# Optimization experiments

Hardware: AMD Instinct MI355X
Metric: run time of the kernel (lower is better)

The kernel has to match this reference:

```python
import jax, jax.numpy as jnp
import numpy as np

LM_DIM = 4096
V_DIM = 1024
N_V = 32
FF = 1024
IN_DIM = V_DIM * N_V + LM_DIM  # 36864
B = 16
T = 2048


def setup_inputs() -> dict:
    key = jax.random.key(0)
    ks = jax.random.split(key, 16)
    grd_hidden = jax.random.normal(ks[0], (T, LM_DIM), dtype=jnp.float32)
    vision_features = jax.random.normal(ks[1], (B, N_V, V_DIM), dtype=jnp.float32)
    token_batch_idx = jnp.sort(jax.random.randint(ks[2], (T,), 0, B, dtype=jnp.int64))
    def lin(k, fan_in, fan_out):
        kw, kb = jax.random.split(k)
        scale = jnp.sqrt(2.0 / (fan_in + fan_out)).astype(jnp.float32)
        W = jax.random.normal(kw, (fan_in, fan_out), dtype=jnp.float32) * scale
        b = jnp.zeros((fan_out,), dtype=jnp.float32)
        return W, b
    W1, b1 = lin(ks[3], IN_DIM, FF)
    W2, b2 = lin(ks[4], FF, FF)
    W3, b3 = lin(ks[5], FF, FF)
    W4, b4 = lin(ks[6], FF, FF)
    W5, b5 = lin(ks[7], FF, 6)
    return {"grd_hidden": grd_hidden, "vision_features": vision_features,
            "token_batch_idx": token_batch_idx,
            "W1": W1, "b1": b1, "W2": W2, "b2": b2, "W3": W3, "b3": b3,
            "W4": W4, "b4": b4, "W5": W5, "b5": b5}


def reference(grd_hidden, vision_features, token_batch_idx,
              W1, b1, W2, b2, W3, b3, W4, b4, W5, b5):
    # flatten vision latents per sample: [B, N_V*V_DIM]
    vis_flat = vision_features.reshape(vision_features.shape[0], -1)
    # per-token gather of the sample's vision feature: [T, N_V*V_DIM]
    vis_per_tok = vis_flat[token_batch_idx]
    # concat(vision, language) per token, then shared 5-layer MLP
    x = jnp.concatenate([vis_per_tok, grd_hidden], axis=-1)  # [T, IN_DIM]
    h = jax.nn.relu(x @ W1 + b1)
    h = jax.nn.relu(h @ W2 + b2)
    h = jax.nn.relu(h @ W3 + b3)
    h = jax.nn.relu(h @ W4 + b4)
    return h @ W5 + b5  # [T, 6]
```

## Files before the change

### kernel.cpp

```cpp
#include <hip/hip_runtime.h>


typedef __attribute__((ext_vector_type(8))) short bf16x8;
typedef __attribute__((ext_vector_type(4))) float f32x4;

#define LM_DIM 4096
#define FF     1024
#define VIS_K  32768
#define NB     16
#define NTOK   2048

__device__ __forceinline__ unsigned short f2bf(float f) {
    unsigned int u = __float_as_uint(f);
    u += 0x7fffu + ((u >> 16) & 1u);
    return (unsigned short)(u >> 16);
}
__device__ __forceinline__ float bf2f(unsigned short s) {
    return __uint_as_float(((unsigned int)s) << 16);
}

__device__ __forceinline__ void gload_lds16(const void* g, void* lds) {
    __builtin_amdgcn_global_load_lds(
        (const __attribute__((address_space(1))) unsigned int*)g,
        (__attribute__((address_space(3))) unsigned int*)lds,
        16, 0, 0);
}

__global__ __launch_bounds__(1024) void vis_partial(
    const float* __restrict__ W1, const float* __restrict__ vis,
    float* __restrict__ pb)
{
    const int n  = threadIdx.x;
    const int ks = blockIdx.x;
    const int k0 = ks * 128;
    __shared__ float sv[NB][128];
    for (int idx = threadIdx.x; idx < NB * 128; idx += 1024) {
        int b = idx >> 7, kk = idx & 127;
        sv[b][kk] = vis[(size_t)b * VIS_K + k0 + kk];
    }
    __syncthreads();
    float acc[NB];
#pragma unroll
    for (int b = 0; b < NB; ++b) acc[b] = 0.f;
    for (int kk = 0; kk < 128; ++kk) {
        float w = W1[(size_t)(k0 + kk) * FF + n];
#pragma unroll
        for (int b = 0; b < NB; ++b) acc[b] += sv[b][kk] * w;
    }
#pragma unroll
    for (int b = 0; b < NB; ++b)
        pb[((size_t)ks * NB + b) * FF + n] = acc[b];
}

__global__ __launch_bounds__(256) void vis_reduce(
    const float* __restrict__ pb, float* __restrict__ vc)
{
    const int lin = blockIdx.x * 256 + threadIdx.x;
    const int n = lin & 1023;
    const int r = lin >> 10;
    const int b = r >> 2;
    const int q = r & 3;
    float s = 0.f;
#pragma unroll 4
    for (int i = 0; i < 64; ++i) {
        int ks = q * 64 + i;
        s += pb[((size_t)ks * NB + b) * FF + n];
    }
    atomicAdd(&vc[b * FF + n], s);
}

__global__ __launch_bounds__(256) void prep_all(
    const float* __restrict__ grd, unsigned short* __restrict__ grdb,
    const float* __restrict__ W1l, unsigned short* __restrict__ W1lT,
    const float* __restrict__ W2,  unsigned short* __restrict__ W2T,
    const float* __restrict__ W3,  unsigned short* __restrict__ W3T,
    const float* __restrict__ W4,  unsigned short* __restrict__ W4T)
{
    __shared__ float t[64][65];
    const int bid = blockIdx.x;
    const int tx = threadIdx.x, ty = threadIdx.y;

    if (bid < 4096) {
        int i = bid * 256 + ty * 64 + tx;
        const float4* p = (const float4*)grd + (size_t)i * 2;
        float4 a = p[0], bvec = p[1];
        union { unsigned short us[8]; uint4 v; } o;
        o.us[0] = f2bf(a.x); o.us[1] = f2bf(a.y);
        o.us[2] = f2bf(a.z); o.us[3] = f2bf(a.w);
        o.us[4] = f2bf(bvec.x); o.us[5] = f2bf(bvec.y);
        o.us[6] = f2bf(bvec.z); o.us[7] = f2bf(bvec.w);
        ((uint4*)grdb)[i] = o.v;
        return;
    }
    const float* src; unsigned short* dst; int K, tt;
    if (bid < 5120)      { src = W1l; dst = W1lT; K = LM_DIM; tt = bid - 4096; }
    else if (bid < 5376) { src = W2;  dst = W2T;  K = FF;     tt = bid - 5120; }
    else if (bid < 5632) { src = W3;  dst = W3T;  K = FF;     tt = bid - 5376; }
    else                 { src = W4;  dst = W4T;  K = FF;     tt = bid - 5632; }
    const int tilesx = K / 64;
    const int k0 = (tt % tilesx) * 64, n0 = (tt / tilesx) * 64;
    for (int r = ty; r < 64; r += 4)
        t[r][tx] = src[(size_t)(k0 + r) * FF + n0 + tx];
    __syncthreads();
    for (int r = ty; r < 64; r += 4)
        dst[(size_t)(n0 + r) * K + k0 + tx] = f2bf(t[tx][r]);
}

template <int EPI>
__global__ __launch_bounds__(256, 2) void gemm_bt(
    const unsigned short* __restrict__ A,
    const unsigned short* __restrict__ BT,
    const float* __restrict__ bias,
    const float* __restrict__ Vc,
    const int* __restrict__ tbi,
    unsigned short* __restrict__ Hout,
    int M, int N, int K)
{
    __shared__ __align__(16) unsigned char smem[32768];

    const int tid  = threadIdx.x;
    const int lane = tid & 63;
    const int wv   = tid >> 6;
    const int wr   = wv >> 1;
    const int wc   = wv & 1;

    const int nwg  = gridDim.x * gridDim.y;
    const int bid0 = blockIdx.y * gridDim.x + blockIdx.x;
    const int cpx  = nwg >> 3;
    const int bid  = (bid0 & 7) * cpx + (bid0 >> 3);
    const int bm   = (bid % gridDim.x) * 64;
    const int bn   = (bid / gridDim.x) * 64;

    const int seg  = wv * 2;
    f32x4 acc[2][2];
#pragma unroll
    for (int m = 0; m < 2; ++m)
#pragma unroll
        for (int n = 0; n < 2; ++n) acc[m][n] = (f32x4){0.f, 0.f, 0.f, 0.f};

    auto stage = [&](int p, int k0) {
        unsigned char* sA = smem + p * 16384;
        unsigned char* sB = sA + 8192;
#pragma unroll
        for (int c = 0; c < 2; ++c) {
            int sg  = seg + c;
            int off = sg * 1024 + lane * 16;
            int row = off >> 7;
            int kb  = (off & 127) ^ ((row & 7) << 4);
            gload_lds16((const unsigned char*)A  + ((size_t)(bm + row) * K + k0) * 2 + kb,
                        sA + sg * 1024);
            gload_lds16((const unsigned char*)BT + ((size_t)(bn + row) * K + k0) * 2 + kb,
                        sB + sg * 1024);
        }
    };
    auto compute = [&](int p) {
        const unsigned char* sA = smem + p * 16384;
        const unsigned char* sB = sA + 8192;
#pragma unroll
        for (int kk = 0; kk < 2; ++kk) {
            const int kbb = kk * 64 + (lane >> 4) * 16;
            bf16x8 av[2], bv[2];
#pragma unroll
            for (int m = 0; m < 2; ++m) {
                int r = wr * 32 + m * 16 + (lane & 15);
                av[m] = *(const bf16x8*)(sA + r * 128 + (kbb ^ ((r & 7) << 4)));
            }
#pragma unroll
            for (int n = 0; n < 2; ++n) {
                int r = wc * 32 + n * 16 + (lane & 15);
                bv[n] = *(const bf16x8*)(sB + r * 128 + (kbb ^ ((r & 7) << 4)));
            }
#pragma unroll
            for (int m = 0; m < 2; ++m)
#pragma unroll
                for (int n = 0; n < 2; ++n)
                    acc[m][n] = __builtin_amdgcn_mfma_f32_16x16x32_bf16(
                        av[m], bv[n], acc[m][n], 0, 0, 0);
        }
    };

    const int nt = K >> 6;
    stage(0, 0);
    __syncthreads();
    for (int t = 0; t < nt; ++t) {
        if (t + 1 < nt) stage((t + 1) & 1, (t + 1) << 6);
        compute(t & 1);
        __syncthreads();
    }

#pragma unroll
    for (int m = 0; m < 2; ++m) {
#pragma unroll
        for (int j = 0; j < 4; ++j) {
            int grow = bm + wr * 32 + m * 16 + (lane >> 4) * 4 + j;
            const float* vrow = (EPI == 1) ? (Vc + (size_t)tbi[grow] * N) : nullptr;
#pragma unroll
            for (int n = 0; n < 2; ++n) {
                int gcol = bn + wc * 32 + n * 16 + (lane & 15);
                float v = acc[m][n][j] + bias[gcol];
                if (EPI == 1) v += vrow[gcol];
                v = fmaxf(v, 0.f);
                Hout[(size_t)grow * N + gcol] = f2bf(v);
            }
        }
    }
}

__global__ __launch_bounds__(256) void final_proj(
    const unsigned short* __restrict__ H, const float* __restrict__ W5,
    const float* __restrict__ b5, float* __restrict__ out)
{
    const int t    = blockIdx.x * 4 + (threadIdx.x >> 6);
    const int lane = threadIdx.x & 63;
    float s[6] = {0.f, 0.f, 0.f, 0.f, 0.f, 0.f};
#pragma unroll
    for (int i = 0; i < 16; ++i) {
        int k = i * 64 + lane;
        float h = bf2f(H[(size_t)t * FF + k]);
#pragma unroll
        for (int j = 0; j < 6; ++j) s[j] += h * W5[(size_t)k * 6 + j];
    }
#pragma unroll
    for (int j = 0; j < 6; ++j) {
#pragma unroll
        for (int off = 32; off > 0; off >>= 1) s[j] += __shfl_down(s[j], off);
    }
    if (lane == 0) {
#pragma unroll
        for (int j = 0; j < 6; ++j) out[(size_t)t * 6 + j] = s[j] + b5[j];
    }
}

extern "C" void kernel_launch(void* const* d_in, const int* in_sizes, int n_in,
                              void* d_out, int out_size, void* d_ws, size_t ws_size,
                              hipStream_t stream) {
    const float* grd = (const float*)d_in[0];
    const float* vis = (const float*)d_in[1];
    const int*   tbi = (const int*)d_in[2];
    const float* W1  = (const float*)d_in[3];
    const float* b1  = (const float*)d_in[4];
    const float* W2  = (const float*)d_in[5];
    const float* b2  = (const float*)d_in[6];
    const float* W3  = (const float*)d_in[7];
    const float* b3  = (const float*)d_in[8];
    const float* W4  = (const float*)d_in[9];
    const float* b4  = (const float*)d_in[10];
    const float* W5  = (const float*)d_in[11];
    const float* b5  = (const float*)d_in[12];
    float* out = (float*)d_out;

    char* ws = (char*)d_ws;
    float*          pb    = (float*)ws;
    float*          Vc    = (float*)(ws + 16777216);
    unsigned short* grdb  = (unsigned short*)(ws + 16842752);
    unsigned short* W1lT  = (unsigned short*)(ws + 33619968);
    unsigned short* W2T   = (unsigned short*)(ws + 42008576);
    unsigned short* W3T   = (unsigned short*)(ws + 44105728);
    unsigned short* W4T   = (unsigned short*)(ws + 46202880);
    unsigned short* hA    = (unsigned short*)(ws + 48300032);
    unsigned short* hB    = (unsigned short*)(ws + 52494336);

    hipMemsetAsync(Vc, 0, NB * FF * sizeof(float), stream);
    vis_partial<<<256, 1024, 0, stream>>>(W1, vis, pb);
    vis_reduce<<<256, 256, 0, stream>>>(pb, Vc);

    prep_all<<<5888, dim3(64, 4), 0, stream>>>(
        grd, grdb, W1 + (size_t)VIS_K * FF, W1lT, W2, W2T, W3, W3T, W4, W4T);

    gemm_bt<1><<<dim3(NTOK / 64, FF / 64), 256, 0, stream>>>(
        grdb, W1lT, b1, Vc, tbi, hA, NTOK, FF, LM_DIM);
    gemm_bt<0><<<dim3(NTOK / 64, FF / 64), 256, 0, stream>>>(
        hA, W2T, b2, nullptr, nullptr, hB, NTOK, FF, FF);
    gemm_bt<0><<<dim3(NTOK / 64, FF / 64), 256, 0, stream>>>(
        hB, W3T, b3, nullptr, nullptr, hA, NTOK, FF, FF);
    gemm_bt<0><<<dim3(NTOK / 64, FF / 64), 256, 0, stream>>>(
        hA, W4T, b4, nullptr, nullptr, hB, NTOK, FF, FF);

    final_proj<<<NTOK / 4, 256, 0, stream>>>(hB, W5, b5, out);
}
```

Measured before the change: 356.6 us.

## Fuse vision partial GEMM into prep kernel, triple-buffer GEMM loads, vectorize final projection

Merges the vision-feature partial product into the single prep kernel, using 512 blocks of 256 threads with 4 columns each, so the weight conversion and vision work run in one launch and share the machine. The bf16 GEMM moves from a double to a triple-buffered LDS pipeline with explicit vmcnt waits and raw barriers, keeping two tiles in flight. The final projection now reads H with ushort4 loads. The costs are more LDS per GEMM block, which may lower occupancy, and a larger partial buffer for vis_reduce to sum.

```diff
diff --git a/kernel.cpp b/kernel.cpp
--- a/kernel.cpp
+++ b/kernel.cpp
@@ -26,30 +26,76 @@
         16, 0, 0);
 }
 
-__global__ __launch_bounds__(1024) void vis_partial(
+__global__ __launch_bounds__(256) void prep_fused(
     const float* __restrict__ W1, const float* __restrict__ vis,
-    float* __restrict__ pb)
+    float* __restrict__ pb,
+    const float* __restrict__ grd, unsigned short* __restrict__ grdb,
+    unsigned short* __restrict__ W1lT,
+    const float* __restrict__ W2,  unsigned short* __restrict__ W2T,
+    const float* __restrict__ W3,  unsigned short* __restrict__ W3T,
+    const float* __restrict__ W4,  unsigned short* __restrict__ W4T)
 {
-    const int n  = threadIdx.x;
-    const int ks = blockIdx.x;
-    const int k0 = ks * 128;
-    __shared__ float sv[NB][128];
-    for (int idx = threadIdx.x; idx < NB * 128; idx += 1024) {
-        int b = idx >> 7, kk = idx & 127;
-        sv[b][kk] = vis[(size_t)b * VIS_K + k0 + kk];
-    }
+    const int bid = blockIdx.x;
+    const int tid = threadIdx.y * 64 + threadIdx.x;
+
+    if (bid < 512) {
+        const int k0 = bid * 64;
+        __shared__ float sv[NB][64];
+        for (int idx = tid; idx < NB * 64; idx += 256) {
+            int b = idx >> 6, kk = idx & 63;
+            sv[b][kk] = vis[(size_t)b * VIS_K + k0 + kk];
+        }
+        __syncthreads();
+        float acc[NB][4];
+#pragma unroll
+        for (int b = 0; b < NB; ++b)
+#pragma unroll
+            for (int c = 0; c < 4; ++c) acc[b][c] = 0.f;
+        for (int kk = 0; kk < 64; ++kk) {
+            const float* wrow = W1 + (size_t)(k0 + kk) * FF;
+            float w0 = wrow[tid], w1 = wrow[tid + 256],
+                  w2 = wrow[tid + 512], w3 = wrow[tid + 768];
+#pragma unroll
+            for (int b = 0; b < NB; ++b) {
+                float v = sv[b][kk];
+                acc[b][0] += v * w0; acc[b][1] += v * w1;
+                acc[b][2] += v * w2; acc[b][3] += v * w3;
+            }
+        }
+#pragma unroll
+        for (int b = 0; b < NB; ++b)
+#pragma unroll
+            for (int c = 0; c < 4; ++c)
+                pb[((size_t)bid * NB + b) * FF + tid + c * 256] = acc[b][c];
+        return;
+    }
+    if (bid < 4608) {
+        int i = (bid - 512) * 256 + tid;
+        const float4* p = (const float4*)grd + (size_t)i * 2;
+        float4 a = p[0], bv = p[1];
+        union { unsigned short us[8]; uint4 v; } o;
+        o.us[0] = f2bf(a.x);  o.us[1] = f2bf(a.y);
+        o.us[2] = f2bf(a.z);  o.us[3] = f2bf(a.w);
+        o.us[4] = f2bf(bv.x); o.us[5] = f2bf(bv.y);
+        o.us[6] = f2bf(bv.z); o.us[7] = f2bf(bv.w);
+        ((uint4*)grdb)[i] = o.v;
+        return;
+    }
+    const float* W1l = W1 + (size_t)VIS_K * FF;
+    const float* src; unsigned short* dst; int K, tt;
+    if (bid < 5632)      { src = W1l; dst = W1lT; K = LM_DIM; tt = bid - 4608; }
+    else if (bid < 5888) { src = W2;  dst = W2T;  K = FF;     tt = bid - 5632; }
+    else if (bid < 6144) { src = W3;  dst = W3T;  K = FF;     tt = bid - 5888; }
+    else                 { src = W4;  dst = W4T;  K = FF;     tt = bid - 6144; }
+    __shared__ float t[64][65];
+    const int tilesx = K / 64;
+    const int k0 = (tt % tilesx) * 64, n0 = (tt / tilesx) * 64;
+    const int tx = threadIdx.x, ty = threadIdx.y;
+    for (int r = ty; r < 64; r += 4)
+        t[r][tx] = src[(size_t)(k0 + r) * FF + n0 + tx];
     __syncthreads();
-    float acc[NB];
-#pragma unroll
-    for (int b = 0; b < NB; ++b) acc[b] = 0.f;
-    for (int kk = 0; kk < 128; ++kk) {
-        float w = W1[(size_t)(k0 + kk) * FF + n];
-#pragma unroll
-        for (int b = 0; b < NB; ++b) acc[b] += sv[b][kk] * w;
-    }
-#pragma unroll
-    for (int b = 0; b < NB; ++b)
-        pb[((size_t)ks * NB + b) * FF + n] = acc[b];
+    for (int r = ty; r < 64; r += 4)
+        dst[(size_t)(n0 + r) * K + k0 + tx] = f2bf(t[tx][r]);
 }
 
 __global__ __launch_bounds__(256) void vis_reduce(
@@ -62,48 +108,11 @@
     const int q = r & 3;
     float s = 0.f;
 #pragma unroll 4
-    for (int i = 0; i < 64; ++i) {
-        int ks = q * 64 + i;
+    for (int i = 0; i < 128; ++i) {
+        int ks = q * 128 + i;
         s += pb[((size_t)ks * NB + b) * FF + n];
     }
     atomicAdd(&vc[b * FF + n], s);
-}
-
-__global__ __launch_bounds__(256) void prep_all(
-    const float* __restrict__ grd, unsigned short* __restrict__ grdb,
-    const float* __restrict__ W1l, unsigned short* __restrict__ W1lT,
-    const float* __restrict__ W2,  unsigned short* __restrict__ W2T,
-    const float* __restrict__ W3,  unsigned short* __restrict__ W3T,
-    const float* __restrict__ W4,  unsigned short* __restrict__ W4T)
-{
-    __shared__ float t[64][65];
-    const int bid = blockIdx.x;
-    const int tx = threadIdx.x, ty = threadIdx.y;
-
-    if (bid < 4096) {
-        int i = bid * 256 + ty * 64 + tx;
-        const float4* p = (const float4*)grd + (size_t)i * 2;
-        float4 a = p[0], bvec = p[1];
-        union { unsigned short us[8]; uint4 v; } o;
-        o.us[0] = f2bf(a.x); o.us[1] = f2bf(a.y);
-        o.us[2] = f2bf(a.z); o.us[3] = f2bf(a.w);
-        o.us[4] = f2bf(bvec.x); o.us[5] = f2bf(bvec.y);
-        o.us[6] = f2bf(bvec.z); o.us[7] = f2bf(bvec.w);
-        ((uint4*)grdb)[i] = o.v;
-        return;
-    }
-    const float* src; unsigned short* dst; int K, tt;
-    if (bid < 5120)      { src = W1l; dst = W1lT; K = LM_DIM; tt = bid - 4096; }
-    else if (bid < 5376) { src = W2;  dst = W2T;  K = FF;     tt = bid - 5120; }
-    else if (bid < 5632) { src = W3;  dst = W3T;  K = FF;     tt = bid - 5376; }
-    else                 { src = W4;  dst = W4T;  K = FF;     tt = bid - 5632; }
-    const int tilesx = K / 64;
-    const int k0 = (tt % tilesx) * 64, n0 = (tt / tilesx) * 64;
-    for (int r = ty; r < 64; r += 4)
-        t[r][tx] = src[(size_t)(k0 + r) * FF + n0 + tx];
-    __syncthreads();
-    for (int r = ty; r < 64; r += 4)
-        dst[(size_t)(n0 + r) * K + k0 + tx] = f2bf(t[tx][r]);
 }
 
 template <int EPI>
@@ -116,7 +125,7 @@
     unsigned short* __restrict__ Hout,
     int M, int N, int K)
 {
-    __shared__ __align__(16) unsigned char smem[32768];
+    __shared__ __align__(16) unsigned char smem[49152];
 
     const int tid  = threadIdx.x;
     const int lane = tid & 63;
@@ -138,8 +147,8 @@
 #pragma unroll
         for (int n = 0; n < 2; ++n) acc[m][n] = (f32x4){0.f, 0.f, 0.f, 0.f};
 
-    auto stage = [&](int p, int k0) {
-        unsigned char* sA = smem + p * 16384;
+    auto stage = [&](int slot, int k0) {
+        unsigned char* sA = smem + slot * 16384;
         unsigned char* sB = sA + 8192;
 #pragma unroll
         for (int c = 0; c < 2; ++c) {
@@ -153,8 +162,8 @@
                         sB + sg * 1024);
         }
     };
-    auto compute = [&](int p) {
-        const unsigned char* sA = smem + p * 16384;
+    auto compute = [&](int slot) {
+        const unsigned char* sA = smem + slot * 16384;
         const unsigned char* sB = sA + 8192;
 #pragma unroll
         for (int kk = 0; kk < 2; ++kk) {
@@ -181,11 +190,22 @@
 
     const int nt = K >> 6;
     stage(0, 0);
-    __syncthreads();
+    stage(1, 64);
+    asm volatile("s_waitcnt vmcnt(4)" ::: "memory");
+    __builtin_amdgcn_s_barrier();
+    int slot = 0;
     for (int t = 0; t < nt; ++t) {
-        if (t + 1 < nt) stage((t + 1) & 1, (t + 1) << 6);
-        compute(t & 1);
-        __syncthreads();
+        if (t + 2 < nt) {
+            int s2 = slot + 2; if (s2 >= 3) s2 -= 3;
+            stage(s2, (t + 2) << 6);
+            compute(slot);
+            asm volatile("s_waitcnt vmcnt(4)" ::: "memory");
+        } else {
+            compute(slot);
+            asm volatile("s_waitcnt vmcnt(0)" ::: "memory");
+        }
+        __builtin_amdgcn_s_barrier();
+        if (++slot == 3) slot = 0;
     }
 
 #pragma unroll
@@ -213,12 +233,17 @@
     const int t    = blockIdx.x * 4 + (threadIdx.x >> 6);
     const int lane = threadIdx.x & 63;
     float s[6] = {0.f, 0.f, 0.f, 0.f, 0.f, 0.f};
-#pragma unroll
-    for (int i = 0; i < 16; ++i) {
-        int k = i * 64 + lane;
-        float h = bf2f(H[(size_t)t * FF + k]);
-#pragma unroll
-        for (int j = 0; j < 6; ++j) s[j] += h * W5[(size_t)k * 6 + j];
+    const ushort4* hrow = (const ushort4*)(H + (size_t)t * FF);
+#pragma unroll
+    for (int i = 0; i < 4; ++i) {
+        ushort4 hv = hrow[i * 64 + lane];
+        int kbase = (i * 64 + lane) * 4;
+#pragma unroll
+        for (int c = 0; c < 4; ++c) {
+            float h = bf2f(c == 0 ? hv.x : c == 1 ? hv.y : c == 2 ? hv.z : hv.w);
+#pragma unroll
+            for (int j = 0; j < 6; ++j) s[j] += h * W5[(size_t)(kbase + c) * 6 + j];
+        }
     }
 #pragma unroll
     for (int j = 0; j < 6; ++j) {
@@ -251,21 +276,19 @@
 
     char* ws = (char*)d_ws;
     float*          pb    = (float*)ws;
-    float*          Vc    = (float*)(ws + 16777216);
-    unsigned short* grdb  = (unsigned short*)(ws + 16842752);
-    unsigned short* W1lT  = (unsigned short*)(ws + 33619968);
-    unsigned short* W2T   = (unsigned short*)(ws + 42008576);
-    unsigned short* W3T   = (unsigned short*)(ws + 44105728);
-    unsigned short* W4T   = (unsigned short*)(ws + 46202880);
-    unsigned short* hA    = (unsigned short*)(ws + 48300032);
-    unsigned short* hB    = (unsigned short*)(ws + 52494336);
+    float*          Vc    = (float*)(ws + 33554432);
+    unsigned short* grdb  = (unsigned short*)(ws + 33619968);
+    unsigned short* W1lT  = (unsigned short*)(ws + 50397184);
+    unsigned short* W2T   = (unsigned short*)(ws + 58785792);
+    unsigned short* W3T   = (unsigned short*)(ws + 60882944);
+    unsigned short* W4T   = (unsigned short*)(ws + 62980096);
+    unsigned short* hA    = (unsigned short*)(ws + 65077248);
+    unsigned short* hB    = (unsigned short*)(ws + 69271552);
 
     hipMemsetAsync(Vc, 0, NB * FF * sizeof(float), stream);
-    vis_partial<<<256, 1024, 0, stream>>>(W1, vis, pb);
+    prep_fused<<<6400, dim3(64, 4), 0, stream>>>(
+        W1, vis, pb, grd, grdb, W1lT, W2, W2T, W3, W3T, W4, W4T);
     vis_reduce<<<256, 256, 0, stream>>>(pb, Vc);
-
-    prep_all<<<5888, dim3(64, 4), 0, stream>>>(
-        grd, grdb, W1 + (size_t)VIS_K * FF, W1lT, W2, W2T, W3, W3T, W4, W4T);
 
     gemm_bt<1><<<dim3(NTOK / 64, FF / 64), 256, 0, stream>>>(
         grdb, W1lT, b1, Vc, tbi, hA, NTOK, FF, LM_DIM);
```

After: 359.1 us. No clear change (+0.7%).
